# Kernel optimization log

Hardware: AMD Instinct MI355X
Metric: run time of the kernel (lower is better)

Reference implementation:

```python
import jax, jax.numpy as jnp
import numpy as np

B, T, D = 4, 4096, 1024
LN_EPS = 1e-5

def _xavier(key, shape, gain=1.0):
    fan_in, fan_out = shape[1], shape[0]
    a = gain * np.sqrt(6.0 / (fan_in + fan_out))
    return jax.random.uniform(key, shape, jnp.float32, -a, a)

def setup_inputs() -> dict:
    key = jax.random.key(0)
    kx, kg, kv, ko = jax.random.split(key, 4)
    # log_decay param init so that softplus(log_decay) == decay_init (0.01)
    log_decay = jnp.asarray(np.log(np.expm1(0.01)), jnp.float32)
    return {
        "x": jax.random.normal(kx, (B, T, D), jnp.float32),
        "ln_w": jnp.ones((D,), jnp.float32),
        "ln_b": jnp.zeros((D,), jnp.float32),
        "gate_w": _xavier(kg, (D, D)),            # torch Linear weight [out, in]
        "gate_b": jnp.zeros((D,), jnp.float32),
        "value_w": _xavier(kv, (D, D), gain=0.01),
        "value_b": jnp.zeros((D,), jnp.float32),
        "out_w": _xavier(ko, (D, D), gain=0.01),
        "out_b": jnp.zeros((D,), jnp.float32),
        "log_decay": log_decay,
    }

def reference(x, ln_w, ln_b, gate_w, gate_b, value_w, value_b, out_w, out_b, log_decay):
    # LayerNorm over last dim
    mu = jnp.mean(x, axis=-1, keepdims=True)
    var = jnp.mean(jnp.square(x - mu), axis=-1, keepdims=True)
    normed = (x - mu) * jax.lax.rsqrt(var + LN_EPS) * ln_w + ln_b
    # gate / value projections (torch Linear: y = x @ W.T + b)
    g = jax.nn.sigmoid(normed @ gate_w.T + gate_b)
    v = normed @ value_w.T + value_b
    # push-pull: cumsum(g*v) - cumsum((1-g)*v) == cumsum((2g-1)*v)
    cumsum = jnp.cumsum((2.0 * g - 1.0) * v, axis=1)
    alpha = jax.nn.softplus(log_decay)
    positions = jnp.arange(T, dtype=jnp.float32)
    decay = jnp.exp(-alpha * positions)[None, :, None]  # [1, T, 1]
    output = cumsum * decay
    return x + (output @ out_w.T + out_b)
```

## Files before the change

kernel.cpp:

```cpp
#include <hip/hip_runtime.h>
#include <hip/hip_bf16.h>

#define BB 4
#define TT 4096
#define DD 1024
#define MM (BB * TT)
#define LN_EPS 1e-5f

typedef __attribute__((ext_vector_type(8))) short bf16x8;
typedef __attribute__((ext_vector_type(4))) float f32x4;

__device__ __forceinline__ float bfbits2f(unsigned short h) {
    return __uint_as_float(((unsigned int)h) << 16);
}
__device__ __forceinline__ unsigned short f2bfbits(float f) {
    __hip_bfloat16 h = __float2bfloat16(f);
    return *reinterpret_cast<unsigned short*>(&h);
}
__device__ __forceinline__ unsigned int pack2(float a, float b) {
    return (unsigned int)f2bfbits(a) | ((unsigned int)f2bfbits(b) << 16);
}

__device__ __forceinline__ void async_copy16(void* lds, const void* g) {
    __builtin_amdgcn_global_load_lds(
        (const __attribute__((address_space(1))) void*)g,
        (__attribute__((address_space(3))) void*)lds,
        16, 0, 0);
}

__global__ __launch_bounds__(256)
void convert_w3(const float* __restrict__ s0, const float* __restrict__ s1,
                const float* __restrict__ s2,
                __hip_bfloat16* __restrict__ d0, __hip_bfloat16* __restrict__ d1,
                __hip_bfloat16* __restrict__ d2)
{
    const int blk = blockIdx.x;
    const int w = blk >> 10;
    const float* src = (w == 0) ? s0 : (w == 1) ? s1 : s2;
    __hip_bfloat16* dst = (w == 0) ? d0 : (w == 1) ? d1 : d2;
    const size_t i = ((size_t)(blk & 1023) * 256 + threadIdx.x) * 4;
    float4 v = *(const float4*)(src + i);
    uint2 o;
    o.x = pack2(v.x, v.y);
    o.y = pack2(v.z, v.w);
    *(uint2*)((unsigned short*)dst + i) = o;
}

__global__ __launch_bounds__(256)
void ln_kernel(const float* __restrict__ x,
               const float* __restrict__ w,
               const float* __restrict__ b,
               __hip_bfloat16* __restrict__ out)
{
    const int wv   = threadIdx.x >> 6;
    const int lane = threadIdx.x & 63;
    const int row  = blockIdx.x * 4 + wv;

    const float* xr = x + (size_t)row * DD + lane * 16;
    float4 v[4];
    #pragma unroll
    for (int i = 0; i < 4; ++i) v[i] = *(const float4*)(xr + i * 4);

    float s = 0.0f, ss = 0.0f;
    #pragma unroll
    for (int i = 0; i < 4; ++i) {
        s  += (v[i].x + v[i].y) + (v[i].z + v[i].w);
        ss += fmaf(v[i].x, v[i].x, fmaf(v[i].y, v[i].y,
              fmaf(v[i].z, v[i].z, v[i].w * v[i].w)));
    }
    #pragma unroll
    for (int o = 32; o > 0; o >>= 1) {
        s  += __shfl_down(s, o);
        ss += __shfl_down(ss, o);
    }
    s  = __shfl(s, 0);
    ss = __shfl(ss, 0);

    const float mu   = s * (1.0f / DD);
    const float var  = ss * (1.0f / DD) - mu * mu;
    const float rstd = rsqrtf(var + LN_EPS);

    unsigned int res[8];
    #pragma unroll
    for (int i = 0; i < 4; ++i) {
        float4 wr = *(const float4*)(w + lane * 16 + i * 4);
        float4 br = *(const float4*)(b + lane * 16 + i * 4);
        float o0 = (v[i].x - mu) * rstd * wr.x + br.x;
        float o1 = (v[i].y - mu) * rstd * wr.y + br.y;
        float o2 = (v[i].z - mu) * rstd * wr.z + br.z;
        float o3 = (v[i].w - mu) * rstd * wr.w + br.w;
        res[i * 2]     = pack2(o0, o1);
        res[i * 2 + 1] = pack2(o2, o3);
    }
    unsigned short* op = (unsigned short*)out + (size_t)row * DD + lane * 16;
    *(uint4*)op       = make_uint4(res[0], res[1], res[2], res[3]);
    *(uint4*)(op + 8) = make_uint4(res[4], res[5], res[6], res[7]);
}

__global__ __launch_bounds__(256, 2)
void dual_gemm_gate(const __hip_bfloat16* __restrict__ A,
                    const __hip_bfloat16* __restrict__ Wg,
                    const __hip_bfloat16* __restrict__ Wv,
                    const float* __restrict__ gb,
                    const float* __restrict__ vb,
                    __hip_bfloat16* __restrict__ U,
                    int M, int N, int K)
{
    constexpr int BK = 32;
    __shared__ short As[128 * BK];
    __shared__ short Bg[128 * BK];
    __shared__ short Bv[128 * BK];

    const int tid  = threadIdx.x;
    const int m0   = blockIdx.x * 128;
    const int n0   = blockIdx.y * 128;
    const int wave = tid >> 6;
    const int lane = tid & 63;
    const int wm   = (wave & 1) * 64;
    const int wn   = (wave >> 1) * 64;
    const int lrow = lane & 15;
    const int kgrp = lane >> 4;

    f32x4 accg[4][4] = {};
    f32x4 accv[4][4] = {};

    const int srow = tid >> 2;
    const int sc   = tid & 3;
    const __hip_bfloat16* ga0 = A  + (size_t)(m0 + srow) * K + sc * 8;
    const __hip_bfloat16* gg0 = Wg + (size_t)(n0 + srow) * K + sc * 8;
    const __hip_bfloat16* gv0 = Wv + (size_t)(n0 + srow) * K + sc * 8;

    for (int k0 = 0; k0 < K; k0 += BK) {
        #pragma unroll
        for (int r = 0; r < 2; ++r) {
            async_copy16(&As[(r * 256 + tid) * 8], ga0 + (size_t)r * 64 * K + k0);
            async_copy16(&Bg[(r * 256 + tid) * 8], gg0 + (size_t)r * 64 * K + k0);
            async_copy16(&Bv[(r * 256 + tid) * 8], gv0 + (size_t)r * 64 * K + k0);
        }
        __builtin_amdgcn_s_waitcnt(0);
        __syncthreads();

        bf16x8 af[4], bgf[4], bvf[4];
        #pragma unroll
        for (int i = 0; i < 4; ++i)
            af[i] = *(const bf16x8*)&As[(wm + i * 16 + lrow) * BK + kgrp * 8];
        #pragma unroll
        for (int j = 0; j < 4; ++j) {
            bgf[j] = *(const bf16x8*)&Bg[(wn + j * 16 + lrow) * BK + kgrp * 8];
            bvf[j] = *(const bf16x8*)&Bv[(wn + j * 16 + lrow) * BK + kgrp * 8];
        }

        #pragma unroll
        for (int i = 0; i < 4; ++i)
            #pragma unroll
            for (int j = 0; j < 4; ++j) {
                accg[i][j] = __builtin_amdgcn_mfma_f32_16x16x32_bf16(
                    bgf[j], af[i], accg[i][j], 0, 0, 0);
                accv[i][j] = __builtin_amdgcn_mfma_f32_16x16x32_bf16(
                    bvf[j], af[i], accv[i][j], 0, 0, 0);
            }
        __syncthreads();
    }

    #pragma unroll
    for (int j = 0; j < 4; ++j) {
        const int nb = n0 + wn + j * 16 + kgrp * 4;
        const float4 gb4 = *(const float4*)(gb + nb);
        const float4 vb4 = *(const float4*)(vb + nb);
        #pragma unroll
        for (int i = 0; i < 4; ++i) {
            const int m = m0 + wm + i * 16 + lrow;
            const float g0 = accg[i][j][0] + gb4.x, v0 = accv[i][j][0] + vb4.x;
            const float g1 = accg[i][j][1] + gb4.y, v1 = accv[i][j][1] + vb4.y;
            const float g2 = accg[i][j][2] + gb4.z, v2 = accv[i][j][2] + vb4.z;
            const float g3 = accg[i][j][3] + gb4.w, v3 = accv[i][j][3] + vb4.w;
            const float u0 = (2.0f / (1.0f + __expf(-g0)) - 1.0f) * v0;
            const float u1 = (2.0f / (1.0f + __expf(-g1)) - 1.0f) * v1;
            const float u2 = (2.0f / (1.0f + __expf(-g2)) - 1.0f) * v2;
            const float u3 = (2.0f / (1.0f + __expf(-g3)) - 1.0f) * v3;
            uint2 o;
            o.x = pack2(u0, u1);
            o.y = pack2(u2, u3);
            *(uint2*)((unsigned short*)U + (size_t)m * N + nb) = o;
        }
    }
}

__global__ __launch_bounds__(256, 2)
void gemm_out(const __hip_bfloat16* __restrict__ A,
              const __hip_bfloat16* __restrict__ W,
              const float* __restrict__ bias,
              const float* __restrict__ X,
              float* __restrict__ C,
              int M, int N, int K)
{
    constexpr int BK = 32;
    __shared__ short As[128 * BK];
    __shared__ short Bs[128 * BK];

    const int tid  = threadIdx.x;
    const int m0   = blockIdx.x * 128;
    const int n0   = blockIdx.y * 128;
    const int wave = tid >> 6;
    const int lane = tid & 63;
    const int wm   = (wave & 1) * 64;
    const int wn   = (wave >> 1) * 64;
    const int lrow = lane & 15;
    const int kgrp = lane >> 4;

    f32x4 acc[4][4] = {};

    const int srow = tid >> 2;
    const int sc   = tid & 3;
    const __hip_bfloat16* ga0 = A + (size_t)(m0 + srow) * K + sc * 8;
    const __hip_bfloat16* gb0 = W + (size_t)(n0 + srow) * K + sc * 8;

    for (int k0 = 0; k0 < K; k0 += BK) {
        #pragma unroll
        for (int r = 0; r < 2; ++r) {
            async_copy16(&As[(r * 256 + tid) * 8], ga0 + (size_t)r * 64 * K + k0);
            async_copy16(&Bs[(r * 256 + tid) * 8], gb0 + (size_t)r * 64 * K + k0);
        }
        __builtin_amdgcn_s_waitcnt(0);
        __syncthreads();

        bf16x8 af[4], bfr[4];
        #pragma unroll
        for (int i = 0; i < 4; ++i)
            af[i] = *(const bf16x8*)&As[(wm + i * 16 + lrow) * BK + kgrp * 8];
        #pragma unroll
        for (int j = 0; j < 4; ++j)
            bfr[j] = *(const bf16x8*)&Bs[(wn + j * 16 + lrow) * BK + kgrp * 8];

        #pragma unroll
        for (int i = 0; i < 4; ++i)
            #pragma unroll
            for (int j = 0; j < 4; ++j)
                acc[i][j] = __builtin_amdgcn_mfma_f32_16x16x32_bf16(
                    bfr[j], af[i], acc[i][j], 0, 0, 0);
        __syncthreads();
    }

    #pragma unroll
    for (int j = 0; j < 4; ++j) {
        const int nb = n0 + wn + j * 16 + kgrp * 4;
        const float4 bv = *(const float4*)(bias + nb);
        #pragma unroll
        for (int i = 0; i < 4; ++i) {
            const int m = m0 + wm + i * 16 + lrow;
            const size_t idx = (size_t)m * N + nb;
            const float4 xv = *(const float4*)(X + idx);
            float4 o;
            o.x = acc[i][j][0] + bv.x + xv.x;
            o.y = acc[i][j][1] + bv.y + xv.y;
            o.z = acc[i][j][2] + bv.z + xv.z;
            o.w = acc[i][j][3] + bv.w + xv.w;
            *(float4*)(C + idx) = o;
        }
    }
}

#define NC 64
#define CL 64

__global__ __launch_bounds__(128)
void scan_partial(const __hip_bfloat16* __restrict__ U, float* __restrict__ Pk)
{
    const int c = blockIdx.x, b = blockIdx.y;
    const int d8 = threadIdx.x * 8;
    const unsigned short* p = (const unsigned short*)U +
        ((size_t)b * TT + (size_t)c * CL) * DD + d8;
    float s[8] = {};
    #pragma unroll 8
    for (int t = 0; t < CL; ++t) {
        uint4 raw = *(const uint4*)(p + (size_t)t * DD);
        unsigned int wds[4] = {raw.x, raw.y, raw.z, raw.w};
        #pragma unroll
        for (int k = 0; k < 4; ++k) {
            s[2 * k]     += bfbits2f((unsigned short)(wds[k] & 0xFFFF));
            s[2 * k + 1] += bfbits2f((unsigned short)(wds[k] >> 16));
        }
    }
    float* o = &Pk[((size_t)b * NC + c) * DD + d8];
    *(float4*)o       = make_float4(s[0], s[1], s[2], s[3]);
    *(float4*)(o + 4) = make_float4(s[4], s[5], s[6], s[7]);
}

__global__ __launch_bounds__(256)
void scan_offsets(float* __restrict__ Pk)
{
    const int col4 = ((int)blockIdx.x * 256 + (int)threadIdx.x) * 4;
    const int b = col4 >> 10;
    const int d = col4 & 1023;
    float r0 = 0, r1 = 0, r2 = 0, r3 = 0;
    float* p = Pk + (size_t)b * NC * DD + d;
    #pragma unroll 8
    for (int c = 0; c < NC; ++c) {
        float4 v = *(float4*)(p + (size_t)c * DD);
        *(float4*)(p + (size_t)c * DD) = make_float4(r0, r1, r2, r3);
        r0 += v.x; r1 += v.y; r2 += v.z; r3 += v.w;
    }
}

__global__ __launch_bounds__(128)
void scan_final(const __hip_bfloat16* __restrict__ U,
                const float* __restrict__ Pk,
                const float* __restrict__ log_decay,
                __hip_bfloat16* __restrict__ S)
{
    const int c = blockIdx.x, b = blockIdx.y;
    const int d8 = threadIdx.x * 8;

    const float ld = log_decay[0];
    const float alpha = log1pf(__expf(ld));
    const float ratio = __expf(-alpha);
    float dec = __expf(-alpha * (float)(c * CL));

    const float* pk = &Pk[((size_t)b * NC + c) * DD + d8];
    float run[8];
    float4 r0 = *(const float4*)pk;
    float4 r1 = *(const float4*)(pk + 4);
    run[0] = r0.x; run[1] = r0.y; run[2] = r0.z; run[3] = r0.w;
    run[4] = r1.x; run[5] = r1.y; run[6] = r1.z; run[7] = r1.w;

    const size_t base = ((size_t)b * TT + (size_t)c * CL) * DD + d8;
    const unsigned short* up = (const unsigned short*)U + base;
    unsigned short* sp = (unsigned short*)S + base;

    #pragma unroll 8
    for (int t = 0; t < CL; ++t) {
        uint4 raw = *(const uint4*)(up + (size_t)t * DD);
        unsigned int wds[4] = {raw.x, raw.y, raw.z, raw.w};
        uint4 o;
        unsigned int* ow = (unsigned int*)&o;
        #pragma unroll
        for (int k = 0; k < 4; ++k) {
            run[2 * k]     += bfbits2f((unsigned short)(wds[k] & 0xFFFF));
            run[2 * k + 1] += bfbits2f((unsigned short)(wds[k] >> 16));
            ow[k] = pack2(run[2 * k] * dec, run[2 * k + 1] * dec);
        }
        *(uint4*)(sp + (size_t)t * DD) = o;
        dec *= ratio;
    }
}

extern "C" void kernel_launch(void* const* d_in, const int* in_sizes, int n_in,
                              void* d_out, int out_size, void* d_ws, size_t ws_size,
                              hipStream_t stream)
{
    const float* x        = (const float*)d_in[0];
    const float* ln_w     = (const float*)d_in[1];
    const float* ln_b     = (const float*)d_in[2];
    const float* gate_w   = (const float*)d_in[3];
    const float* gate_b   = (const float*)d_in[4];
    const float* value_w  = (const float*)d_in[5];
    const float* value_b  = (const float*)d_in[6];
    const float* out_w    = (const float*)d_in[7];
    const float* out_b    = (const float*)d_in[8];
    const float* log_dec  = (const float*)d_in[9];
    float* out = (float*)d_out;

    char* ws = (char*)d_ws;
    const size_t MB = 1024 * 1024;
    __hip_bfloat16* normed = (__hip_bfloat16*)(ws);
    __hip_bfloat16* S      = (__hip_bfloat16*)(ws);
    float*          Pk     = (float*)(ws + 32 * MB);
    __hip_bfloat16* Wg16   = (__hip_bfloat16*)(ws + 33 * MB);
    __hip_bfloat16* Wv16   = (__hip_bfloat16*)(ws + 35 * MB);
    __hip_bfloat16* Wo16   = (__hip_bfloat16*)(ws + 37 * MB);
    __hip_bfloat16* U      = (__hip_bfloat16*)d_out;

    convert_w3<<<dim3(3072), dim3(256), 0, stream>>>(
        gate_w, value_w, out_w, Wg16, Wv16, Wo16);

    ln_kernel<<<dim3(MM / 4), dim3(256), 0, stream>>>(x, ln_w, ln_b, normed);

    dual_gemm_gate<<<dim3(MM / 128, DD / 128), dim3(256), 0, stream>>>(
        normed, Wg16, Wv16, gate_b, value_b, U, MM, DD, DD);

    scan_partial<<<dim3(NC, BB), dim3(128), 0, stream>>>(U, Pk);
    scan_offsets<<<dim3(4), dim3(256), 0, stream>>>(Pk);
    scan_final<<<dim3(NC, BB), dim3(128), 0, stream>>>(U, Pk, log_dec, S);

    gemm_out<<<dim3(MM / 128, DD / 128), dim3(256), 0, stream>>>(
        S, Wo16, out_b, x, out, MM, DD, DD);
}
```

Measured before the change: 319.6 us.

## Double GEMM K-tile to 64 with XOR-swizzled LDS layout

Both GEMM kernels now stage 64-wide K tiles instead of 32, so each load/sync round feeds twice as many MFMAs, halving the number of barriers and waitcnt stalls per K loop. The global-to-LDS copy places 16-byte chunks at positions XORed by row, and the fragment reads apply the same swizzle to avoid LDS bank conflicts on the wider rows. LDS use doubles (48KB for the dual-gate kernel), which may limit how many blocks fit per CU alongside launch bounds of 2.

```diff
diff --git a/kernel.cpp b/kernel.cpp
--- a/kernel.cpp
+++ b/kernel.cpp
@@ -106,7 +106,7 @@
                     __hip_bfloat16* __restrict__ U,
                     int M, int N, int K)
 {
-    constexpr int BK = 32;
+    constexpr int BK = 64;
     __shared__ short As[128 * BK];
     __shared__ short Bg[128 * BK];
     __shared__ short Bv[128 * BK];
@@ -120,45 +120,56 @@
     const int wn   = (wave >> 1) * 64;
     const int lrow = lane & 15;
     const int kgrp = lane >> 4;
+    const int swz  = lrow & 7;
 
     f32x4 accg[4][4] = {};
     f32x4 accv[4][4] = {};
 
-    const int srow = tid >> 2;
-    const int sc   = tid & 3;
-    const __hip_bfloat16* ga0 = A  + (size_t)(m0 + srow) * K + sc * 8;
-    const __hip_bfloat16* gg0 = Wg + (size_t)(n0 + srow) * K + sc * 8;
-    const __hip_bfloat16* gv0 = Wv + (size_t)(n0 + srow) * K + sc * 8;
+    const __hip_bfloat16* gA[4];
+    const __hip_bfloat16* gG[4];
+    const __hip_bfloat16* gV[4];
+    #pragma unroll
+    for (int r = 0; r < 4; ++r) {
+        const int slot = r * 256 + tid;
+        const int srow = slot >> 3;
+        const int gcc  = (slot & 7) ^ (srow & 7);
+        gA[r] = A  + (size_t)(m0 + srow) * K + gcc * 8;
+        gG[r] = Wg + (size_t)(n0 + srow) * K + gcc * 8;
+        gV[r] = Wv + (size_t)(n0 + srow) * K + gcc * 8;
+    }
 
     for (int k0 = 0; k0 < K; k0 += BK) {
         #pragma unroll
-        for (int r = 0; r < 2; ++r) {
-            async_copy16(&As[(r * 256 + tid) * 8], ga0 + (size_t)r * 64 * K + k0);
-            async_copy16(&Bg[(r * 256 + tid) * 8], gg0 + (size_t)r * 64 * K + k0);
-            async_copy16(&Bv[(r * 256 + tid) * 8], gv0 + (size_t)r * 64 * K + k0);
+        for (int r = 0; r < 4; ++r) {
+            async_copy16(&As[(r * 256 + tid) * 8], gA[r] + k0);
+            async_copy16(&Bg[(r * 256 + tid) * 8], gG[r] + k0);
+            async_copy16(&Bv[(r * 256 + tid) * 8], gV[r] + k0);
         }
         __builtin_amdgcn_s_waitcnt(0);
         __syncthreads();
 
-        bf16x8 af[4], bgf[4], bvf[4];
-        #pragma unroll
-        for (int i = 0; i < 4; ++i)
-            af[i] = *(const bf16x8*)&As[(wm + i * 16 + lrow) * BK + kgrp * 8];
-        #pragma unroll
-        for (int j = 0; j < 4; ++j) {
-            bgf[j] = *(const bf16x8*)&Bg[(wn + j * 16 + lrow) * BK + kgrp * 8];
-            bvf[j] = *(const bf16x8*)&Bv[(wn + j * 16 + lrow) * BK + kgrp * 8];
-        }
-
-        #pragma unroll
-        for (int i = 0; i < 4; ++i)
+        #pragma unroll
+        for (int ks = 0; ks < 2; ++ks) {
+            const int co = ((ks * 4 + kgrp) ^ swz) * 8;
+            bf16x8 af[4], bgf[4], bvf[4];
+            #pragma unroll
+            for (int i = 0; i < 4; ++i)
+                af[i] = *(const bf16x8*)&As[(wm + i * 16 + lrow) * BK + co];
             #pragma unroll
             for (int j = 0; j < 4; ++j) {
-                accg[i][j] = __builtin_amdgcn_mfma_f32_16x16x32_bf16(
-                    bgf[j], af[i], accg[i][j], 0, 0, 0);
-                accv[i][j] = __builtin_amdgcn_mfma_f32_16x16x32_bf16(
-                    bvf[j], af[i], accv[i][j], 0, 0, 0);
+                bgf[j] = *(const bf16x8*)&Bg[(wn + j * 16 + lrow) * BK + co];
+                bvf[j] = *(const bf16x8*)&Bv[(wn + j * 16 + lrow) * BK + co];
             }
+            #pragma unroll
+            for (int i = 0; i < 4; ++i)
+                #pragma unroll
+                for (int j = 0; j < 4; ++j) {
+                    accg[i][j] = __builtin_amdgcn_mfma_f32_16x16x32_bf16(
+                        bgf[j], af[i], accg[i][j], 0, 0, 0);
+                    accv[i][j] = __builtin_amdgcn_mfma_f32_16x16x32_bf16(
+                        bvf[j], af[i], accv[i][j], 0, 0, 0);
+                }
+        }
         __syncthreads();
     }
 
@@ -194,7 +205,7 @@
               float* __restrict__ C,
               int M, int N, int K)
 {
-    constexpr int BK = 32;
+    constexpr int BK = 64;
     __shared__ short As[128 * BK];
     __shared__ short Bs[128 * BK];
 
@@ -207,37 +218,47 @@
     const int wn   = (wave >> 1) * 64;
     const int lrow = lane & 15;
     const int kgrp = lane >> 4;
+    const int swz  = lrow & 7;
 
     f32x4 acc[4][4] = {};
 
-    const int srow = tid >> 2;
-    const int sc   = tid & 3;
-    const __hip_bfloat16* ga0 = A + (size_t)(m0 + srow) * K + sc * 8;
-    const __hip_bfloat16* gb0 = W + (size_t)(n0 + srow) * K + sc * 8;
+    const __hip_bfloat16* gA[4];
+    const __hip_bfloat16* gB[4];
+    #pragma unroll
+    for (int r = 0; r < 4; ++r) {
+        const int slot = r * 256 + tid;
+        const int srow = slot >> 3;
+        const int gcc  = (slot & 7) ^ (srow & 7);
+        gA[r] = A + (size_t)(m0 + srow) * K + gcc * 8;
+        gB[r] = W + (size_t)(n0 + srow) * K + gcc * 8;
+    }
 
     for (int k0 = 0; k0 < K; k0 += BK) {
         #pragma unroll
-        for (int r = 0; r < 2; ++r) {
-            async_copy16(&As[(r * 256 + tid) * 8], ga0 + (size_t)r * 64 * K + k0);
-            async_copy16(&Bs[(r * 256 + tid) * 8], gb0 + (size_t)r * 64 * K + k0);
+        for (int r = 0; r < 4; ++r) {
+            async_copy16(&As[(r * 256 + tid) * 8], gA[r] + k0);
+            async_copy16(&Bs[(r * 256 + tid) * 8], gB[r] + k0);
         }
         __builtin_amdgcn_s_waitcnt(0);
         __syncthreads();
 
-        bf16x8 af[4], bfr[4];
-        #pragma unroll
-        for (int i = 0; i < 4; ++i)
-            af[i] = *(const bf16x8*)&As[(wm + i * 16 + lrow) * BK + kgrp * 8];
-        #pragma unroll
-        for (int j = 0; j < 4; ++j)
-            bfr[j] = *(const bf16x8*)&Bs[(wn + j * 16 + lrow) * BK + kgrp * 8];
-
-        #pragma unroll
-        for (int i = 0; i < 4; ++i)
+        #pragma unroll
+        for (int ks = 0; ks < 2; ++ks) {
+            const int co = ((ks * 4 + kgrp) ^ swz) * 8;
+            bf16x8 af[4], bfr[4];
+            #pragma unroll
+            for (int i = 0; i < 4; ++i)
+                af[i] = *(const bf16x8*)&As[(wm + i * 16 + lrow) * BK + co];
             #pragma unroll
             for (int j = 0; j < 4; ++j)
-                acc[i][j] = __builtin_amdgcn_mfma_f32_16x16x32_bf16(
-                    bfr[j], af[i], acc[i][j], 0, 0, 0);
+                bfr[j] = *(const bf16x8*)&Bs[(wn + j * 16 + lrow) * BK + co];
+            #pragma unroll
+            for (int i = 0; i < 4; ++i)
+                #pragma unroll
+                for (int j = 0; j < 4; ++j)
+                    acc[i][j] = __builtin_amdgcn_mfma_f32_16x16x32_bf16(
+                        bfr[j], af[i], acc[i][j], 0, 0, 0);
+        }
         __syncthreads();
     }
 
```

Result: faster. 297.3 us (-7.0%).
